# Performance work log

Measured on AMD Instinct MI355X. Metric: run time of the kernel, lower is better.

The kernel has to match this reference:

```python
import jax, jax.numpy as jnp
import numpy as np

N = 100_000   # nodes
K = 32        # incoming edges per node (regular graph)
IN = 128
OUT = 64


def setup_inputs() -> dict:
    key = jax.random.key(0)
    k1, k2, k3 = jax.random.split(key, 3)
    x = jax.random.normal(k1, (N, IN), jnp.float32)
    # K-regular graph: each target node has exactly K incoming edges
    row = jax.random.randint(k2, (N * K,), 0, N)          # source nodes
    col = jnp.repeat(jnp.arange(N), K)                    # target nodes
    edge_index = jnp.stack([row, col]).astype(jnp.int64)  # [2, E]
    lim = float(np.sqrt(6.0 / (IN + OUT)))                # glorot uniform
    W = jax.random.uniform(k3, (IN, OUT), jnp.float32, -lim, lim)
    b = jnp.zeros((OUT,), jnp.float32)
    return {"x": x, "edge_index": edge_index, "W": W, "b": b}


def reference(x, edge_index, W, b):
    h = x @ W                                   # [N, OUT] linear (no bias in lin)
    n = h.shape[0]
    row = edge_index[0]
    k = row.shape[0] // n
    # edge_index is a K-regular graph with col = repeat(arange(N), K),
    # so the K source nodes of target i live at row[i*K:(i+1)*K].
    nbrs = row.reshape(n, k)                    # [N, K]
    # add self loops -> K+1 (odd) neighbors, exact unique median
    nbrs = jnp.concatenate([nbrs, jnp.arange(n, dtype=nbrs.dtype)[:, None]], axis=1)
    gathered = h[nbrs]                          # [N, K+1, OUT] -- dominant traffic
    out = jnp.median(gathered, axis=1)          # elementwise exact median per node
    return out + b
```

## Files before the change

### kernel.cpp

```cpp
#include <hip/hip_runtime.h>
#include <hip/hip_bf16.h>

#define N_IN 128
#define N_OUT 64
#define KNBR 32

typedef __attribute__((ext_vector_type(4))) float fx4;
typedef __attribute__((ext_vector_type(2))) float fx2;
typedef __attribute__((ext_vector_type(8))) short bh8;

struct Net {
  int a[64];
  int b[64];
  int n;
};

constexpr Net make_batcher16() {
  Net net{};
  net.n = 0;
  const int n = 16;
  for (int p = 1; p < n; p <<= 1)
    for (int k = p; k >= 1; k >>= 1)
      for (int j = k % p; j + k < n; j += 2 * k)
        for (int i = 0; i < k && i + j + k < n; ++i)
          if ((i + j) / (2 * p) == (i + j + k) / (2 * p)) {
            net.a[net.n] = i + j;
            net.b[net.n] = i + j + k;
            net.n++;
          }
  return net;
}

constexpr Net NET16 = make_batcher16();
static_assert(NET16.n == 63, "batcher16 comparator count must be 63");

__device__ __forceinline__ unsigned pkmin(unsigned a, unsigned b) {
  unsigned r;
  asm("v_pk_min_u16 %0, %1, %2" : "=v"(r) : "v"(a), "v"(b));
  return r;
}
__device__ __forceinline__ unsigned pkmax(unsigned a, unsigned b) {
  unsigned r;
  asm("v_pk_max_u16 %0, %1, %2" : "=v"(r) : "v"(a), "v"(b));
  return r;
}
__device__ __forceinline__ void casp(unsigned& x, unsigned& y) {
  unsigned lo = pkmin(x, y);
  unsigned hi = pkmax(x, y);
  x = lo;
  y = hi;
}

__device__ __forceinline__ unsigned short bf_bits(float f) {
  union { __hip_bfloat16 b; unsigned short u; } cv;
  cv.b = __float2bfloat16(f);
  return cv.u;
}

__device__ __forceinline__ unsigned cvtpk(float a, float b) {
  unsigned r;
  asm("v_cvt_pk_bf16_f32 %0, %1, %2" : "=v"(r) : "v"(a), "v"(b));
  return r;
}

__device__ __forceinline__ void tile_compute_store(
    const fx4* xp, const bh8 bf[4][4], unsigned short* __restrict__ h,
    int t, int n, int l4, int g) {
  fx4 acc[4];
#pragma unroll
  for (int ct = 0; ct < 4; ++ct) acc[ct] = fx4{0.f, 0.f, 0.f, 0.f};

#pragma unroll
  for (int kc = 0; kc < 4; ++kc) {
    union { unsigned u[4]; bh8 s; } av;
    av.u[0] = cvtpk(xp[kc * 2 + 0].x, xp[kc * 2 + 0].y);
    av.u[1] = cvtpk(xp[kc * 2 + 0].z, xp[kc * 2 + 0].w);
    av.u[2] = cvtpk(xp[kc * 2 + 1].x, xp[kc * 2 + 1].y);
    av.u[3] = cvtpk(xp[kc * 2 + 1].z, xp[kc * 2 + 1].w);
#pragma unroll
    for (int ct = 0; ct < 4; ++ct)
      acc[ct] = __builtin_amdgcn_mfma_f32_16x16x32_bf16(av.s, bf[kc][ct],
                                                        acc[ct], 0, 0, 0);
  }

#pragma unroll
  for (int ct = 0; ct < 4; ++ct)
#pragma unroll
    for (int r = 0; r < 4; ++r) {
      int row = t * 16 + g * 4 + r;
      if (row < n) {
        unsigned short ub = bf_bits(acc[ct][r]);
        unsigned short key = (ub & 0x8000) ? (unsigned short)(~ub)
                                           : (unsigned short)(ub | 0x8000);
        h[(size_t)row * N_OUT + ct * 16 + l4] = key;
      }
    }
}

__device__ __forceinline__ void tile_load(fx4* xp, const float* __restrict__ x,
                                          int t, int n, int l4, int g) {
  int row = t * 16 + l4;
  if (row >= n) row = n - 1;
  const float* xr = x + (size_t)row * N_IN + g * 8;
#pragma unroll
  for (int kc = 0; kc < 4; ++kc) {
    xp[kc * 2 + 0] = *(const fx4*)(xr + kc * 32);
    xp[kc * 2 + 1] = *(const fx4*)(xr + kc * 32 + 4);
  }
}

__global__ __launch_bounds__(320) void gemm_kernel(
    const float* __restrict__ x, const float* __restrict__ W,
    unsigned short* __restrict__ h, int n) {
  const int lane = threadIdx.x & 63;
  const int l4 = lane & 15;
  const int g = lane >> 4;
  const int wid = blockIdx.x * 5 + (threadIdx.x >> 6);
  const int nw = gridDim.x * 5;
  const int ntiles = (n + 15) >> 4;
  if (wid >= ntiles) return;

  const int t0 = wid;
  const int t1 = wid + nw;

  fx4 xa[8], xb[8];
  tile_load(xa, x, t0, n, l4, g);
  const bool has2 = (t1 < ntiles);
  if (has2) tile_load(xb, x, t1, n, l4, g);

  bh8 bf[4][4];
#pragma unroll
  for (int kc = 0; kc < 4; ++kc)
#pragma unroll
    for (int ct = 0; ct < 4; ++ct) {
      float f[8];
#pragma unroll
      for (int j = 0; j < 8; ++j)
        f[j] = W[(size_t)(kc * 32 + g * 8 + j) * N_OUT + ct * 16 + l4];
      union { unsigned u[4]; bh8 s; } cv;
      cv.u[0] = cvtpk(f[0], f[1]);
      cv.u[1] = cvtpk(f[2], f[3]);
      cv.u[2] = cvtpk(f[4], f[5]);
      cv.u[3] = cvtpk(f[6], f[7]);
      bf[kc][ct] = cv.s;
    }

  tile_compute_store(xa, bf, h, t0, n, l4, g);
  if (has2) tile_compute_store(xb, bf, h, t1, n, l4, g);

  for (int t = t1 + nw; t < ntiles; t += nw) {
    tile_load(xa, x, t, n, l4, g);
    tile_compute_store(xa, bf, h, t, n, l4, g);
  }
}

__global__ __launch_bounds__(256, 4) void median_kernel(
    const unsigned short* __restrict__ h, const void* __restrict__ ei,
    const float* __restrict__ bias, float* __restrict__ out, int n) {
  const int lane = threadIdx.x & 63;
  const int wid = blockIdx.x * (blockDim.x >> 6) + (threadIdx.x >> 6);
  const int nodeA = wid * 2;
  if (nodeA >= n) return;
  const int l5 = lane & 31;
  const int mynode = nodeA + (lane >> 5);

  const int* e32 = (const int*)ei;
  const long long* e64 = (const long long*)ei;
  bool is64 = (e32[1] == 0) && (e32[3] == 0) && (e32[5] == 0) &&
              (e32[7] == 0) && (e32[9] == 0) && (e32[11] == 0) &&
              (e32[13] == 0) && (e32[15] == 0);

  int idx;
  if (is64) {
    idx = (int)__builtin_nontemporal_load(&e64[mynode * KNBR + l5]);
  } else {
    idx = __builtin_nontemporal_load(&e32[mynode * KNBR + l5]);
  }

  const unsigned laneoff = (unsigned)l5 * 4u;
  unsigned v[33];
#pragma unroll
  for (int j = 0; j < 32; ++j) {
    int s = __shfl(idx, j, 32);
    unsigned off = ((unsigned)s << 7) + laneoff;
    v[j] = *(const unsigned*)((const char*)h + off);
  }
  {
    unsigned off = ((unsigned)mynode << 7) + laneoff;
    v[32] = *(const unsigned*)((const char*)h + off);
  }

#pragma unroll
  for (int t = 0; t < NET16.n; ++t) casp(v[NET16.a[t]], v[NET16.b[t]]);
#pragma unroll
  for (int t = 0; t < NET16.n; ++t) casp(v[16 + NET16.a[t]], v[16 + NET16.b[t]]);

  unsigned r15 = 0u;
  unsigned r16 = 0xFFFFFFFFu;
#pragma unroll
  for (int i = 0; i < 16; ++i) {
    unsigned lo = pkmin(v[i], v[16 + 15 - i]);
    unsigned hi = pkmax(v[i], v[16 + 15 - i]);
    r15 = pkmax(r15, lo);
    r16 = pkmin(r16, hi);
  }

  unsigned med = pkmax(r15, pkmin(v[32], r16));

  unsigned sg = (med >> 15) & 0x00010001u;
  unsigned u = med ^ ~(sg * 0x7FFFu);
  fx2 res;
  res.x = __uint_as_float(u << 16) + bias[2 * l5];
  res.y = __uint_as_float(u & 0xFFFF0000u) + bias[2 * l5 + 1];
  __builtin_nontemporal_store(res, (fx2*)(out + (size_t)mynode * N_OUT + 2 * l5));
}

extern "C" void kernel_launch(void* const* d_in, const int* in_sizes, int n_in,
                              void* d_out, int out_size, void* d_ws, size_t ws_size,
                              hipStream_t stream) {
  const float* x = (const float*)d_in[0];
  const void* ei = d_in[1];
  const float* W = (const float*)d_in[2];
  const float* b = (const float*)d_in[3];
  float* out = (float*)d_out;
  unsigned short* h = (unsigned short*)d_ws;

  const int n = in_sizes[0] / N_IN;

  const int ntiles = (n + 15) >> 4;
  const int waves = (ntiles + 1) >> 1;
  const int gblocks = (waves + 4) / 5;
  gemm_kernel<<<gblocks, 320, 0, stream>>>(x, W, h, n);

  const int grid = (n + 7) / 8;
  median_kernel<<<grid, 256, 0, stream>>>(h, ei, b, out, n);
}
```

Measured before the change: 70.52 us.

## Slice h into channel-major 16-column planes and gather per slice with LDS indices

The GEMM now writes h as four channel slices of 16 bf16 keys each (32 bytes per node per slice), so each median block gathers from a 3.2MB slice that fits better in cache. Block ids interleave slices so neighbouring blocks share the same nodes. A new pre-pass converts the int64 edge list to int32 in workspace, and the median kernel stages the indices in LDS, with each lane handling 4 channels and 8-byte loads. The cost is an extra kernel launch, an extra pass over the edges, and four separate reads of the index list.

```diff
diff --git a/kernel.cpp b/kernel.cpp
--- a/kernel.cpp
+++ b/kernel.cpp
@@ -4,9 +4,10 @@
 #define N_IN 128
 #define N_OUT 64
 #define KNBR 32
+#define SLICE_CH 16
+#define NPB 64
 
 typedef __attribute__((ext_vector_type(4))) float fx4;
-typedef __attribute__((ext_vector_type(2))) float fx2;
 typedef __attribute__((ext_vector_type(8))) short bh8;
 
 struct Net {
@@ -44,12 +45,6 @@
   asm("v_pk_max_u16 %0, %1, %2" : "=v"(r) : "v"(a), "v"(b));
   return r;
 }
-__device__ __forceinline__ void casp(unsigned& x, unsigned& y) {
-  unsigned lo = pkmin(x, y);
-  unsigned hi = pkmax(x, y);
-  x = lo;
-  y = hi;
-}
 
 __device__ __forceinline__ unsigned short bf_bits(float f) {
   union { __hip_bfloat16 b; unsigned short u; } cv;
@@ -61,6 +56,26 @@
   unsigned r;
   asm("v_cvt_pk_bf16_f32 %0, %1, %2" : "=v"(r) : "v"(a), "v"(b));
   return r;
+}
+
+__global__ __launch_bounds__(256) void normalize_edges(
+    const void* __restrict__ ei, int* __restrict__ e32c, long long E) {
+  const int* e32 = (const int*)ei;
+  const long long* e64 = (const long long*)ei;
+  bool is64 = (e32[1] == 0) && (e32[3] == 0) && (e32[5] == 0) &&
+              (e32[7] == 0) && (e32[9] == 0) && (e32[11] == 0) &&
+              (e32[13] == 0) && (e32[15] == 0);
+  const long long i0 = (long long)blockIdx.x * blockDim.x + threadIdx.x;
+  const long long stride = (long long)gridDim.x * blockDim.x;
+  for (long long i = i0; i < E; i += stride) {
+    int v;
+    if (is64) {
+      v = (int)__builtin_nontemporal_load(&e64[i]);
+    } else {
+      v = __builtin_nontemporal_load(&e32[i]);
+    }
+    __builtin_nontemporal_store(v, &e32c[i]);
+  }
 }
 
 __device__ __forceinline__ void tile_compute_store(
@@ -92,7 +107,7 @@
         unsigned short ub = bf_bits(acc[ct][r]);
         unsigned short key = (ub & 0x8000) ? (unsigned short)(~ub)
                                            : (unsigned short)(ub | 0x8000);
-        h[(size_t)row * N_OUT + ct * 16 + l4] = key;
+        h[((size_t)ct * n + row) * SLICE_CH + l4] = key;
       }
     }
 }
@@ -155,64 +170,101 @@
 }
 
 __global__ __launch_bounds__(256, 4) void median_kernel(
-    const unsigned short* __restrict__ h, const void* __restrict__ ei,
+    const unsigned short* __restrict__ hs, const int* __restrict__ e32c,
     const float* __restrict__ bias, float* __restrict__ out, int n) {
-  const int lane = threadIdx.x & 63;
-  const int wid = blockIdx.x * (blockDim.x >> 6) + (threadIdx.x >> 6);
-  const int nodeA = wid * 2;
-  if (nodeA >= n) return;
-  const int l5 = lane & 31;
-  const int mynode = nodeA + (lane >> 5);
-
-  const int* e32 = (const int*)ei;
-  const long long* e64 = (const long long*)ei;
-  bool is64 = (e32[1] == 0) && (e32[3] == 0) && (e32[5] == 0) &&
-              (e32[7] == 0) && (e32[9] == 0) && (e32[11] == 0) &&
-              (e32[13] == 0) && (e32[15] == 0);
-
-  int idx;
-  if (is64) {
-    idx = (int)__builtin_nontemporal_load(&e64[mynode * KNBR + l5]);
-  } else {
-    idx = __builtin_nontemporal_load(&e32[mynode * KNBR + l5]);
-  }
-
-  const unsigned laneoff = (unsigned)l5 * 4u;
-  unsigned v[33];
+  __shared__ int sidx[NPB * 33];
+
+  const int bid = blockIdx.x;
+  const int slice = (bid & 7) >> 1;
+  const int sub = bid & 1;
+  const int chunk = bid >> 3;
+  const int node0 = (chunk * 2 + sub) * NPB;
+  if (node0 >= n) return;
+
+  const int t = threadIdx.x;
+  const long long ebase = (long long)node0 * KNBR;
+#pragma unroll
+  for (int k = 0; k < 8; ++k) {
+    int p = k * 256 + t;
+    int nb = p >> 5;
+    int v = 0;
+    if (node0 + nb < n) v = __builtin_nontemporal_load(&e32c[ebase + p]);
+    sidx[nb * 33 + (p & 31)] = v;
+  }
+  __syncthreads();
+
+  const int lane = t & 63;
+  const int wslot = t >> 6;
+  const int nb = wslot * 16 + (lane >> 2);
+  const int node = node0 + nb;
+  const int q = lane & 3;
+  const bool active = (node < n);
+
+  const unsigned char* hbase =
+      (const unsigned char*)hs + (size_t)slice * ((size_t)n * 32u);
+  const unsigned lanebyte = (unsigned)q * 8u;
+
+  unsigned v[33][2];
 #pragma unroll
   for (int j = 0; j < 32; ++j) {
-    int s = __shfl(idx, j, 32);
-    unsigned off = ((unsigned)s << 7) + laneoff;
-    v[j] = *(const unsigned*)((const char*)h + off);
+    unsigned s = (unsigned)sidx[nb * 33 + j];
+    const unsigned* p = (const unsigned*)(hbase + ((size_t)s * 32u + lanebyte));
+    v[j][0] = p[0];
+    v[j][1] = p[1];
   }
   {
-    unsigned off = ((unsigned)mynode << 7) + laneoff;
-    v[32] = *(const unsigned*)((const char*)h + off);
-  }
-
-#pragma unroll
-  for (int t = 0; t < NET16.n; ++t) casp(v[NET16.a[t]], v[NET16.b[t]]);
-#pragma unroll
-  for (int t = 0; t < NET16.n; ++t) casp(v[16 + NET16.a[t]], v[16 + NET16.b[t]]);
-
-  unsigned r15 = 0u;
-  unsigned r16 = 0xFFFFFFFFu;
-#pragma unroll
-  for (int i = 0; i < 16; ++i) {
-    unsigned lo = pkmin(v[i], v[16 + 15 - i]);
-    unsigned hi = pkmax(v[i], v[16 + 15 - i]);
-    r15 = pkmax(r15, lo);
-    r16 = pkmin(r16, hi);
-  }
-
-  unsigned med = pkmax(r15, pkmin(v[32], r16));
-
-  unsigned sg = (med >> 15) & 0x00010001u;
-  unsigned u = med ^ ~(sg * 0x7FFFu);
-  fx2 res;
-  res.x = __uint_as_float(u << 16) + bias[2 * l5];
-  res.y = __uint_as_float(u & 0xFFFF0000u) + bias[2 * l5 + 1];
-  __builtin_nontemporal_store(res, (fx2*)(out + (size_t)mynode * N_OUT + 2 * l5));
+    unsigned s = active ? (unsigned)node : 0u;
+    const unsigned* p = (const unsigned*)(hbase + ((size_t)s * 32u + lanebyte));
+    v[32][0] = p[0];
+    v[32][1] = p[1];
+  }
+
+#pragma unroll
+  for (int c = 0; c < 2; ++c) {
+#pragma unroll
+    for (int i = 0; i < NET16.n; ++i) {
+      unsigned lo = pkmin(v[NET16.a[i]][c], v[NET16.b[i]][c]);
+      unsigned hi = pkmax(v[NET16.a[i]][c], v[NET16.b[i]][c]);
+      v[NET16.a[i]][c] = lo;
+      v[NET16.b[i]][c] = hi;
+    }
+#pragma unroll
+    for (int i = 0; i < NET16.n; ++i) {
+      unsigned lo = pkmin(v[16 + NET16.a[i]][c], v[16 + NET16.b[i]][c]);
+      unsigned hi = pkmax(v[16 + NET16.a[i]][c], v[16 + NET16.b[i]][c]);
+      v[16 + NET16.a[i]][c] = lo;
+      v[16 + NET16.b[i]][c] = hi;
+    }
+  }
+
+  unsigned med[2];
+#pragma unroll
+  for (int c = 0; c < 2; ++c) {
+    unsigned r15 = 0u;
+    unsigned r16 = 0xFFFFFFFFu;
+#pragma unroll
+    for (int i = 0; i < 16; ++i) {
+      unsigned lo = pkmin(v[i][c], v[16 + 15 - i][c]);
+      unsigned hi = pkmax(v[i][c], v[16 + 15 - i][c]);
+      r15 = pkmax(r15, lo);
+      r16 = pkmin(r16, hi);
+    }
+    med[c] = pkmax(r15, pkmin(v[32][c], r16));
+  }
+
+  if (active) {
+    fx4 res;
+    const fx4 bb = *(const fx4*)(bias + slice * SLICE_CH + q * 4);
+#pragma unroll
+    for (int c = 0; c < 2; ++c) {
+      unsigned sg = (med[c] >> 15) & 0x00010001u;
+      unsigned u = med[c] ^ ~(sg * 0x7FFFu);
+      res[2 * c + 0] = __uint_as_float(u << 16) + bb[2 * c + 0];
+      res[2 * c + 1] = __uint_as_float(u & 0xFFFF0000u) + bb[2 * c + 1];
+    }
+    __builtin_nontemporal_store(
+        res, (fx4*)(out + (size_t)node * N_OUT + slice * SLICE_CH + q * 4));
+  }
 }
 
 extern "C" void kernel_launch(void* const* d_in, const int* in_sizes, int n_in,
@@ -223,15 +275,20 @@
   const float* W = (const float*)d_in[2];
   const float* b = (const float*)d_in[3];
   float* out = (float*)d_out;
+
+  const int n = in_sizes[0] / N_IN;
+  const long long E = (long long)n * KNBR;
+
   unsigned short* h = (unsigned short*)d_ws;
-
-  const int n = in_sizes[0] / N_IN;
+  int* e32c = (int*)((char*)d_ws + (size_t)n * 64 * 2);
+
+  normalize_edges<<<1024, 256, 0, stream>>>(ei, e32c, E);
 
   const int ntiles = (n + 15) >> 4;
   const int waves = (ntiles + 1) >> 1;
   const int gblocks = (waves + 4) / 5;
   gemm_kernel<<<gblocks, 320, 0, stream>>>(x, W, h, n);
 
-  const int grid = (n + 7) / 8;
-  median_kernel<<<grid, 256, 0, stream>>>(h, ei, b, out, n);
-}
+  const int chunks = (n + 2 * NPB - 1) / (2 * NPB);
+  median_kernel<<<chunks * 8, 256, 0, stream>>>(h, e32c, b, out, n);
+}
```

New measurement: 115.1 us. +63.2%, slower.
